# Kernel tuning notes

Hardware: AMD Instinct MI355X
Metric: run time of the kernel (lower is better)

## Reference

```python
import jax, jax.numpy as jnp
import numpy as np

NUM_NODES = 100000
NUM_REL = 237
D = 200            # entity_out_dim_1 * nheads_GAT_1 = 100*2
C = 50             # conv_out_channels
B = 8192           # batch of (h, r, t) triples


def setup_inputs() -> dict:
    key = jax.random.key(0)
    ks = jax.random.split(key, 8)
    heads = jax.random.randint(ks[0], (B, 1), 0, NUM_NODES)
    rels = jax.random.randint(ks[1], (B, 1), 0, NUM_REL)
    tails = jax.random.randint(ks[2], (B, 1), 0, NUM_NODES)
    batch_inputs = jnp.concatenate([heads, rels, tails], axis=1).astype(jnp.int64)
    return {
        "batch_inputs": batch_inputs,
        "final_entity_embeddings": jax.random.normal(ks[3], (NUM_NODES, D), jnp.float32),
        "final_relation_embeddings": jax.random.normal(ks[4], (NUM_REL, D), jnp.float32),
        "W_ent2rel": jax.random.normal(ks[5], (NUM_REL, D, D), jnp.float32) * (1.0 / np.sqrt(D)),
        "conv_w": jax.random.normal(ks[6], (C, 3), jnp.float32) * 0.5,
        "conv_b": jnp.zeros((C,), jnp.float32),
        "fc_w": jax.random.normal(ks[7], (1, C * D), jnp.float32) * (1.0 / np.sqrt(C * D)),
        "fc_b": jnp.zeros((1,), jnp.float32),
    }


def reference(batch_inputs, final_entity_embeddings, final_relation_embeddings,
              W_ent2rel, conv_w, conv_b, fc_w, fc_b):
    h_idx, r_idx, t_idx = batch_inputs[:, 0], batch_inputs[:, 1], batch_inputs[:, 2]
    src = final_entity_embeddings[h_idx]        # [B, D]
    rel = final_relation_embeddings[r_idx]      # [B, D]
    tail = final_entity_embeddings[t_idx]       # [B, D]
    W = W_ent2rel[r_idx]                        # [B, D, D] per-edge relation transform
    # bmm([B,1,D], [B,D,D]) -> [B,1,D], nonlinearity_ent2rel = tanh
    src = jnp.tanh(jnp.einsum('bd,bde->be', src, W))
    tail = jnp.tanh(jnp.einsum('bd,bde->be', tail, W))
    # ConvKB: stack triple as length-3 sequence, Conv2d kernel (1,3) over seq
    stacked = jnp.stack([src, rel, tail], axis=1)            # [B, 3, D]
    conv = jnp.einsum('bkd,ck->bcd', stacked, conv_w) + conv_b[None, :, None]
    conv = jax.nn.relu(conv)                                  # dropout p=0.0 (eval)
    flat = conv.reshape(conv.shape[0], -1)                    # [B, C*D] (C-major, matches torch view)
    out = flat @ fc_w.T + fc_b                                # [B, 1]
    return out
```

## Files before the change

### kernel.cpp

```cpp
#include <hip/hip_runtime.h>
#include <hip/hip_bf16.h>
#include <math.h>

#define DDIM 200
#define D4   50
#define CCH  50
#define NREL 237
#define MAXE 4
#define MAXR 8
#define AROWS 16
#define NT   256
#define KT   7
#define KTKG 28
#define NCOLP 208
#define OSTRIDE 204
#define PACK_UNITS (NREL * KTKG * NCOLP)

typedef __attribute__((ext_vector_type(8))) short bf16x8;
typedef __attribute__((ext_vector_type(4))) float f32x4;

__device__ __forceinline__ uint f2bf(float x) {
    __hip_bfloat16 h = __float2bfloat16(x);
    return (uint)*reinterpret_cast<ushort*>(&h);
}

__device__ __forceinline__ float fast_tanh(float x) {
    const float xc = fminf(fmaxf(x, -20.f), 20.f);
    const float e  = __expf(2.f * xc);
    return 1.f - __fdividef(2.f, e + 1.f);
}

__global__ __launch_bounds__(1024) void prep_kernel(
    const float* __restrict__ W, ushort* __restrict__ Wpk, int do_pack,
    const int* __restrict__ bi, int B, int nblk,
    int* __restrict__ perm, int* __restrict__ blk_r,
    int* __restrict__ blk_start, int* __restrict__ blk_cnt)
{
    const int tid = threadIdx.x;

    if (blockIdx.x != 0) {
        if (!do_pack) return;
        const int u = (blockIdx.x - 1) * 1024 + tid;
        if (u >= PACK_UNITS) return;
        const int col  = u % NCOLP;
        const int rk   = u / NCOLP;
        const int ktkg = rk % KTKG;
        const int r    = rk / KTKG;
        const int k0   = ktkg * 8;
        uint4 pk = {0u, 0u, 0u, 0u};
        if (col < DDIM) {
            const float* base = W + (size_t)r * DDIM * DDIM + col;
            uint vv[8];
            #pragma unroll
            for (int j = 0; j < 8; ++j) {
                const int k = k0 + j;
                vv[j] = (k < DDIM) ? f2bf(base[(size_t)k * DDIM]) : 0u;
            }
            pk.x = vv[0] | (vv[1] << 16);
            pk.y = vv[2] | (vv[3] << 16);
            pk.z = vv[4] | (vv[5] << 16);
            pk.w = vv[6] | (vv[7] << 16);
        }
        *(uint4*)&Wpk[(size_t)u * 8] = pk;
        return;
    }

    __shared__ int hist[NREL];
    __shared__ int offs[NREL];
    __shared__ int wsum[16], wsum2[16];
    const int lane = tid & 63;
    const int w    = tid >> 6;

    if (tid < NREL) hist[tid] = 0;
    __syncthreads();
    for (int i = tid; i < B; i += 1024)
        atomicAdd(&hist[bi[i * 3 + 1]], 1);
    __syncthreads();

    const int v  = (tid < NREL) ? hist[tid] : 0;
    const int v2 = (tid < NREL) ? (v + MAXE - 1) / MAXE : 0;
    int s = v, s2 = v2;
    #pragma unroll
    for (int off = 1; off < 64; off <<= 1) {
        const int u  = __shfl_up(s,  off, 64);
        const int u2 = __shfl_up(s2, off, 64);
        if (lane >= off) { s += u; s2 += u2; }
    }
    if (lane == 63) { wsum[w] = s; wsum2[w] = s2; }
    __syncthreads();
    int base = 0, base2 = 0;
    for (int i = 0; i < w; ++i) { base += wsum[i]; base2 += wsum2[i]; }
    const int my_off  = base  + s  - v;
    const int my_boff = base2 + s2 - v2;
    if (tid < NREL) offs[tid] = my_off;
    __syncthreads();

    for (int i = tid; i < nblk; i += 1024) blk_cnt[i] = 0;
    if (tid < NREL && v > 0) {
        const int nb = (v + MAXE - 1) / MAXE;
        const int cb = v / nb, ext = v - cb * nb;
        int pos = my_off;
        for (int j = 0; j < nb; ++j) {
            const int c = cb + (j < ext ? 1 : 0);
            blk_r[my_boff + j]     = tid;
            blk_start[my_boff + j] = pos;
            blk_cnt[my_boff + j]   = c;
            pos += c;
        }
    }
    __syncthreads();
    for (int i = tid; i < B; i += 1024) {
        const int pos = atomicAdd(&offs[bi[i * 3 + 1]], 1);
        perm[pos] = i;
    }
}

template <bool PACKED>
__global__ __launch_bounds__(NT) void spkbgat_mfma_kernel(
    const int*   __restrict__ bi,
    const float* __restrict__ ent,
    const float* __restrict__ rel_emb,
    const float* __restrict__ W,
    const ushort* __restrict__ Wpk,
    const float* __restrict__ conv_w,
    const float* __restrict__ conv_b,
    const float* __restrict__ fc_w,
    const float* __restrict__ fc_b,
    const int*   __restrict__ perm,
    const int*   __restrict__ blk_r,
    const int*   __restrict__ blk_start,
    const int*   __restrict__ blk_cnt,
    int nblk,
    float*       __restrict__ out)
{
    __shared__ __align__(16) ushort Ash[KTKG * AROWS * 8];
    __shared__ __align__(16) float  Osh[MAXR][OSTRIDE];
    __shared__ __align__(16) float4 rl4[D4];
    __shared__ __align__(16) float  cwb[CCH][4];
    __shared__ int eid_lds[MAXR];
    __shared__ int bix_lds[MAXE];

    const int tid  = threadIdx.x;
    const int w    = tid >> 6;
    const int lane = tid & 63;
    const int l16  = lane & 15;
    const int kg   = lane >> 4;

    const int bid = blockIdx.x;
    const int q = nblk >> 3, rmd = nblk & 7;
    const int xcd = bid & 7, idx = bid >> 3;
    const int gidx = (xcd < rmd ? xcd * (q + 1) : rmd * (q + 1) + (xcd - rmd) * q) + idx;

    const int cnt = blk_cnt[gidx];
    if (cnt == 0) return;

    const int r     = blk_r[gidx];
    const int start = blk_start[gidx];
    const int rows  = 2 * cnt;

    if (tid < CCH) {
        cwb[tid][0] = conv_w[tid * 3 + 0];
        cwb[tid][1] = conv_w[tid * 3 + 1];
        cwb[tid][2] = conv_w[tid * 3 + 2];
        cwb[tid][3] = conv_b[tid];
    }
    if (tid < D4) rl4[tid] = ((const float4*)rel_emb)[r * D4 + tid];
    if (tid < MAXE) {
        const int b = (tid < cnt) ? perm[start + tid] : -1;
        bix_lds[tid] = b;
        const int bb = (b >= 0) ? b : 0;
        eid_lds[2 * tid]     = bi[3 * bb + 0];
        eid_lds[2 * tid + 1] = bi[3 * bb + 2];
    }
    __syncthreads();

    for (int u = tid; u < KTKG * AROWS; u += NT) {
        const int row  = u & (AROWS - 1);
        const int ktkg = u >> 4;
        uint4 pk = {0u, 0u, 0u, 0u};
        if (ktkg < 25 && row < rows) {
            const float* xp = ent + (size_t)eid_lds[row] * DDIM + ktkg * 8;
            const float4 x0 = *(const float4*)xp;
            const float4 x1 = *(const float4*)(xp + 4);
            pk.x = f2bf(x0.x) | (f2bf(x0.y) << 16);
            pk.y = f2bf(x0.z) | (f2bf(x0.w) << 16);
            pk.z = f2bf(x1.x) | (f2bf(x1.y) << 16);
            pk.w = f2bf(x1.z) | (f2bf(x1.w) << 16);
        }
        *(uint4*)&Ash[u * 8] = pk;
    }
    __syncthreads();

    const int nslots = (w == 0) ? 4 : 3;
    const float*  __restrict__ Wr = W + (size_t)r * DDIM * DDIM;
    const ushort* __restrict__ Wp = Wpk + (size_t)r * KTKG * NCOLP * 8;
    f32x4 acc[4];
    #pragma unroll
    for (int s = 0; s < 4; ++s) acc[s] = (f32x4){0.f, 0.f, 0.f, 0.f};

    for (int kt = 0; kt < KT; ++kt) {
        const int ktkg = kt * 4 + kg;
        const bf16x8 a0 = *(const bf16x8*)&Ash[(ktkg * AROWS + l16) * 8];
        #pragma unroll
        for (int s = 0; s < 4; ++s) {
            if (s < nslots) {
                const int col = (w + 4 * s) * 16 + l16;
                bf16x8 bf;
                if (PACKED) {
                    bf = *(const bf16x8*)&Wp[((size_t)ktkg * NCOLP + col) * 8];
                } else {
                    const int k0 = ktkg * 8;
                    #pragma unroll
                    for (int j = 0; j < 8; ++j) {
                        const int k = k0 + j;
                        const float vv = (k < DDIM && col < DDIM) ? Wr[k * DDIM + col] : 0.f;
                        bf[j] = (short)f2bf(vv);
                    }
                }
                acc[s] = __builtin_amdgcn_mfma_f32_16x16x32_bf16(a0, bf, acc[s], 0, 0, 0);
            }
        }
    }

    #pragma unroll
    for (int s = 0; s < 4; ++s) {
        if (s < nslots) {
            const int gcol = (w + 4 * s) * 16 + l16;
            if (gcol < DDIM) {
                #pragma unroll
                for (int v = 0; v < 4; ++v) {
                    const int grow = kg * 4 + v;
                    if (grow < rows)
                        Osh[grow][gcol] = fast_tanh(acc[s][v]);
                }
            }
        }
    }
    __syncthreads();

    float4 sumv = {0.f, 0.f, 0.f, 0.f};
    const bool live = (w < cnt);
    if (lane < D4 && live) {
        const float4 rv = rl4[lane];
        const float4 se = *(const float4*)&Osh[2 * w][4 * lane];
        const float4 te = *(const float4*)&Osh[2 * w + 1][4 * lane];
        for (int c = 0; c < CCH; ++c) {
            const float4 cw  = *(const float4*)&cwb[c][0];
            const float4 fc4 = ((const float4*)fc_w)[c * D4 + lane];
            const float v0 = fmaf(cw.x, se.x, fmaf(cw.y, rv.x, fmaf(cw.z, te.x, cw.w)));
            const float v1 = fmaf(cw.x, se.y, fmaf(cw.y, rv.y, fmaf(cw.z, te.y, cw.w)));
            const float v2 = fmaf(cw.x, se.z, fmaf(cw.y, rv.z, fmaf(cw.z, te.z, cw.w)));
            const float v3 = fmaf(cw.x, se.w, fmaf(cw.y, rv.w, fmaf(cw.z, te.w, cw.w)));
            sumv.x = fmaf(fmaxf(v0, 0.f), fc4.x, sumv.x);
            sumv.y = fmaf(fmaxf(v1, 0.f), fc4.y, sumv.y);
            sumv.z = fmaf(fmaxf(v2, 0.f), fc4.z, sumv.z);
            sumv.w = fmaf(fmaxf(v3, 0.f), fc4.w, sumv.w);
        }
    }
    float sum = (sumv.x + sumv.y) + (sumv.z + sumv.w);
    #pragma unroll
    for (int off = 32; off; off >>= 1)
        sum += __shfl_down(sum, off, 64);
    if (lane == 0 && live) out[bix_lds[w]] = sum + fc_b[0];
}

extern "C" void kernel_launch(void* const* d_in, const int* in_sizes, int n_in,
                              void* d_out, int out_size, void* d_ws, size_t ws_size,
                              hipStream_t stream) {
    const int*   bi      = (const int*)  d_in[0];
    const float* ent     = (const float*)d_in[1];
    const float* rel_emb = (const float*)d_in[2];
    const float* W       = (const float*)d_in[3];
    const float* conv_w  = (const float*)d_in[4];
    const float* conv_b  = (const float*)d_in[5];
    const float* fc_w    = (const float*)d_in[6];
    const float* fc_b    = (const float*)d_in[7];
    float*       out     = (float*)d_out;

    const int B    = in_sizes[0] / 3;
    const int nblk = NREL + (B + MAXE - 1) / MAXE;

    int* perm      = (int*)d_ws;
    int* blk_r     = perm + B;
    int* blk_start = blk_r + nblk;
    int* blk_cnt   = blk_start + nblk;

    const size_t meta_bytes = (size_t)(B + 3 * nblk) * sizeof(int);
    const size_t pk_off     = (meta_bytes + 255) & ~(size_t)255;
    const size_t need       = pk_off + (size_t)PACK_UNITS * 16;
    const bool   use_packed = (ws_size >= need);
    ushort* Wpk = (ushort*)((char*)d_ws + pk_off);

    const int prep_blocks = 1 + (PACK_UNITS + 1023) / 1024;
    prep_kernel<<<prep_blocks, 1024, 0, stream>>>(
        W, Wpk, use_packed ? 1 : 0, bi, B, nblk, perm, blk_r, blk_start, blk_cnt);

    if (use_packed) {
        spkbgat_mfma_kernel<true><<<nblk, NT, 0, stream>>>(
            bi, ent, rel_emb, W, Wpk, conv_w, conv_b, fc_w, fc_b,
            perm, blk_r, blk_start, blk_cnt, nblk, out);
    } else {
        spkbgat_mfma_kernel<false><<<nblk, NT, 0, stream>>>(
            bi, ent, rel_emb, W, Wpk, conv_w, conv_b, fc_w, fc_b,
            perm, blk_r, blk_start, blk_cnt, nblk, out);
    }
}
```

Before: 57.41 us.

## Split fused GEMM+epilogue into separate GEMM and epilogue kernels with larger tiles

Splits the per-relation kernel into two. The GEMM kernel now handles up to 16 triples (32 rows, two MFMA M-tiles) per block, loads entity rows straight into registers instead of staging them in LDS, and writes the tanh outputs as bf16 to a workspace buffer. A new epilogue kernel stages fc_w in LDS and computes the ConvKB reduction for two triples per wave. The aim is to load each relation's W slice fewer times, cut the number of blocks, and drop the per-block global fc_w reads. In exchange it adds a kernel launch, a global round trip for the intermediates, and a bf16 rounding step on the tanh outputs.

```diff
diff --git a/kernel.cpp b/kernel.cpp
--- a/kernel.cpp
+++ b/kernel.cpp
@@ -6,15 +6,14 @@
 #define D4   50
 #define CCH  50
 #define NREL 237
-#define MAXE 4
-#define MAXR 8
-#define AROWS 16
+#define MAXE 16
 #define NT   256
 #define KT   7
 #define KTKG 28
 #define NCOLP 208
-#define OSTRIDE 204
+#define ZSTR 208
 #define PACK_UNITS (NREL * KTKG * NCOLP)
+#define EPB_EPI 8
 
 typedef __attribute__((ext_vector_type(8))) short bf16x8;
 typedef __attribute__((ext_vector_type(4))) float f32x4;
@@ -23,7 +22,9 @@
     __hip_bfloat16 h = __float2bfloat16(x);
     return (uint)*reinterpret_cast<ushort*>(&h);
 }
-
+__device__ __forceinline__ float bf2f(ushort u) {
+    return __uint_as_float((uint)u << 16);
+}
 __device__ __forceinline__ float fast_tanh(float x) {
     const float xc = fminf(fmaxf(x, -20.f), 20.f);
     const float e  = __expf(2.f * xc);
@@ -34,7 +35,8 @@
     const float* __restrict__ W, ushort* __restrict__ Wpk, int do_pack,
     const int* __restrict__ bi, int B, int nblk,
     int* __restrict__ perm, int* __restrict__ blk_r,
-    int* __restrict__ blk_start, int* __restrict__ blk_cnt)
+    int* __restrict__ blk_start, int* __restrict__ blk_cnt,
+    int* __restrict__ eidArr, int* __restrict__ prb, int* __restrict__ prr)
 {
     const int tid = threadIdx.x;
 
@@ -113,33 +115,28 @@
         const int pos = atomicAdd(&offs[bi[i * 3 + 1]], 1);
         perm[pos] = i;
     }
+    __syncthreads();
+    for (int p = tid; p < B; p += 1024) {
+        const int b = perm[p];
+        eidArr[2 * p]     = bi[3 * b + 0];
+        eidArr[2 * p + 1] = bi[3 * b + 2];
+        prb[p] = b;
+        prr[p] = bi[3 * b + 1];
+    }
 }
 
 template <bool PACKED>
-__global__ __launch_bounds__(NT) void spkbgat_mfma_kernel(
-    const int*   __restrict__ bi,
-    const float* __restrict__ ent,
-    const float* __restrict__ rel_emb,
-    const float* __restrict__ W,
+__global__ __launch_bounds__(NT) void gemm_kernel(
+    const float*  __restrict__ ent,
+    const float*  __restrict__ W,
     const ushort* __restrict__ Wpk,
-    const float* __restrict__ conv_w,
-    const float* __restrict__ conv_b,
-    const float* __restrict__ fc_w,
-    const float* __restrict__ fc_b,
-    const int*   __restrict__ perm,
-    const int*   __restrict__ blk_r,
-    const int*   __restrict__ blk_start,
-    const int*   __restrict__ blk_cnt,
+    const int*    __restrict__ blk_r,
+    const int*    __restrict__ blk_start,
+    const int*    __restrict__ blk_cnt,
+    const int*    __restrict__ eidArr,
     int nblk,
-    float*       __restrict__ out)
+    ushort*       __restrict__ Zpk)
 {
-    __shared__ __align__(16) ushort Ash[KTKG * AROWS * 8];
-    __shared__ __align__(16) float  Osh[MAXR][OSTRIDE];
-    __shared__ __align__(16) float4 rl4[D4];
-    __shared__ __align__(16) float  cwb[CCH][4];
-    __shared__ int eid_lds[MAXR];
-    __shared__ int bix_lds[MAXE];
-
     const int tid  = threadIdx.x;
     const int w    = tid >> 6;
     const int lane = tid & 63;
@@ -153,115 +150,178 @@
 
     const int cnt = blk_cnt[gidx];
     if (cnt == 0) return;
-
     const int r     = blk_r[gidx];
     const int start = blk_start[gidx];
     const int rows  = 2 * cnt;
 
+    const int row0 = l16, row1 = 16 + l16;
+    const int e0 = (row0 < rows) ? eidArr[2 * start + row0] : 0;
+    const int e1 = (row1 < rows) ? eidArr[2 * start + row1] : 0;
+    const float* __restrict__ xp0 = ent + (size_t)e0 * DDIM;
+    const float* __restrict__ xp1 = ent + (size_t)e1 * DDIM;
+
+    const ushort* __restrict__ Wp = Wpk + (size_t)r * KTKG * NCOLP * 8;
+    const float*  __restrict__ Wr = W + (size_t)r * DDIM * DDIM;
+    const int nslots = (w == 0) ? 4 : 3;
+
+    f32x4 acc[2][4];
+    #pragma unroll
+    for (int mt = 0; mt < 2; ++mt)
+        #pragma unroll
+        for (int s = 0; s < 4; ++s)
+            acc[mt][s] = (f32x4){0.f, 0.f, 0.f, 0.f};
+
+    #pragma unroll 2
+    for (int kt = 0; kt < KT; ++kt) {
+        const int ktkg = kt * 4 + kg;
+        const int k0   = ktkg * 8;
+        uint4 pa0 = {0u, 0u, 0u, 0u}, pa1 = {0u, 0u, 0u, 0u};
+        if (ktkg < 25) {
+            const float4 a = *(const float4*)(xp0 + k0);
+            const float4 b = *(const float4*)(xp0 + k0 + 4);
+            pa0.x = f2bf(a.x) | (f2bf(a.y) << 16);
+            pa0.y = f2bf(a.z) | (f2bf(a.w) << 16);
+            pa0.z = f2bf(b.x) | (f2bf(b.y) << 16);
+            pa0.w = f2bf(b.z) | (f2bf(b.w) << 16);
+            const float4 c = *(const float4*)(xp1 + k0);
+            const float4 d = *(const float4*)(xp1 + k0 + 4);
+            pa1.x = f2bf(c.x) | (f2bf(c.y) << 16);
+            pa1.y = f2bf(c.z) | (f2bf(c.w) << 16);
+            pa1.z = f2bf(d.x) | (f2bf(d.y) << 16);
+            pa1.w = f2bf(d.z) | (f2bf(d.w) << 16);
+        }
+        const bf16x8 a0 = *reinterpret_cast<const bf16x8*>(&pa0);
+        const bf16x8 a1 = *reinterpret_cast<const bf16x8*>(&pa1);
+        #pragma unroll
+        for (int s = 0; s < 4; ++s) {
+            if (s < nslots) {
+                const int col = (w + 4 * s) * 16 + l16;
+                bf16x8 bfr;
+                if (PACKED) {
+                    bfr = *(const bf16x8*)&Wp[((size_t)ktkg * NCOLP + col) * 8];
+                } else {
+                    #pragma unroll
+                    for (int j = 0; j < 8; ++j) {
+                        const int k = k0 + j;
+                        const float vv = (k < DDIM && col < DDIM) ? Wr[k * DDIM + col] : 0.f;
+                        bfr[j] = (short)f2bf(vv);
+                    }
+                }
+                acc[0][s] = __builtin_amdgcn_mfma_f32_16x16x32_bf16(a0, bfr, acc[0][s], 0, 0, 0);
+                acc[1][s] = __builtin_amdgcn_mfma_f32_16x16x32_bf16(a1, bfr, acc[1][s], 0, 0, 0);
+            }
+        }
+    }
+
+    #pragma unroll
+    for (int mt = 0; mt < 2; ++mt) {
+        #pragma unroll
+        for (int s = 0; s < 4; ++s) {
+            if (s < nslots) {
+                const int col = (w + 4 * s) * 16 + l16;
+                #pragma unroll
+                for (int v = 0; v < 4; ++v) {
+                    const int grow = 16 * mt + kg * 4 + v;
+                    if (grow < rows)
+                        Zpk[(size_t)(2 * start + grow) * ZSTR + col] =
+                            (ushort)f2bf(fast_tanh(acc[mt][s][v]));
+                }
+            }
+        }
+    }
+}
+
+__global__ __launch_bounds__(NT) void epi_kernel(
+    const ushort* __restrict__ Zpk,
+    const float*  __restrict__ rel_emb,
+    const float*  __restrict__ conv_w,
+    const float*  __restrict__ conv_b,
+    const float*  __restrict__ fc_w,
+    const float*  __restrict__ fc_b,
+    const int*    __restrict__ prb,
+    const int*    __restrict__ prr,
+    int B,
+    float*        __restrict__ out)
+{
+    __shared__ __align__(16) float4 fsh[CCH * D4];
+    __shared__ __align__(16) float  cwb[CCH][4];
+
+    const int tid  = threadIdx.x;
+    const int w    = tid >> 6;
+    const int lane = tid & 63;
+
+    for (int i = tid; i < CCH * D4; i += NT) fsh[i] = ((const float4*)fc_w)[i];
     if (tid < CCH) {
         cwb[tid][0] = conv_w[tid * 3 + 0];
         cwb[tid][1] = conv_w[tid * 3 + 1];
         cwb[tid][2] = conv_w[tid * 3 + 2];
         cwb[tid][3] = conv_b[tid];
     }
-    if (tid < D4) rl4[tid] = ((const float4*)rel_emb)[r * D4 + tid];
-    if (tid < MAXE) {
-        const int b = (tid < cnt) ? perm[start + tid] : -1;
-        bix_lds[tid] = b;
-        const int bb = (b >= 0) ? b : 0;
-        eid_lds[2 * tid]     = bi[3 * bb + 0];
-        eid_lds[2 * tid + 1] = bi[3 * bb + 2];
-    }
-    __syncthreads();
-
-    for (int u = tid; u < KTKG * AROWS; u += NT) {
-        const int row  = u & (AROWS - 1);
-        const int ktkg = u >> 4;
-        uint4 pk = {0u, 0u, 0u, 0u};
-        if (ktkg < 25 && row < rows) {
-            const float* xp = ent + (size_t)eid_lds[row] * DDIM + ktkg * 8;
-            const float4 x0 = *(const float4*)xp;
-            const float4 x1 = *(const float4*)(xp + 4);
-            pk.x = f2bf(x0.x) | (f2bf(x0.y) << 16);
-            pk.y = f2bf(x0.z) | (f2bf(x0.w) << 16);
-            pk.z = f2bf(x1.x) | (f2bf(x1.y) << 16);
-            pk.w = f2bf(x1.z) | (f2bf(x1.w) << 16);
-        }
-        *(uint4*)&Ash[u * 8] = pk;
-    }
-    __syncthreads();
-
-    const int nslots = (w == 0) ? 4 : 3;
-    const float*  __restrict__ Wr = W + (size_t)r * DDIM * DDIM;
-    const ushort* __restrict__ Wp = Wpk + (size_t)r * KTKG * NCOLP * 8;
-    f32x4 acc[4];
+    __syncthreads();
+
+    const int p0 = blockIdx.x * EPB_EPI + w * 2;
+    const int p1 = p0 + 1;
+    const bool l0 = (p0 < B), l1 = (p1 < B);
+    const int b0 = l0 ? prb[p0] : 0;
+    const int b1 = l1 ? prb[p1] : 0;
+    const int r0 = l0 ? prr[p0] : 0;
+    const int r1 = l1 ? prr[p1] : 0;
+
+    float4 a0 = {0.f, 0.f, 0.f, 0.f}, a1 = {0.f, 0.f, 0.f, 0.f};
+    if (lane < D4) {
+        float4 se0 = {0,0,0,0}, te0 = {0,0,0,0}, rv0 = {0,0,0,0};
+        float4 se1 = {0,0,0,0}, te1 = {0,0,0,0}, rv1 = {0,0,0,0};
+        if (l0) {
+            rv0 = *(const float4*)&rel_emb[r0 * DDIM + 4 * lane];
+            const ushort4 su = *(const ushort4*)&Zpk[(size_t)(2 * p0) * ZSTR + 4 * lane];
+            const ushort4 tu = *(const ushort4*)&Zpk[(size_t)(2 * p0 + 1) * ZSTR + 4 * lane];
+            se0 = (float4){bf2f(su.x), bf2f(su.y), bf2f(su.z), bf2f(su.w)};
+            te0 = (float4){bf2f(tu.x), bf2f(tu.y), bf2f(tu.z), bf2f(tu.w)};
+        }
+        if (l1) {
+            rv1 = *(const float4*)&rel_emb[r1 * DDIM + 4 * lane];
+            const ushort4 su = *(const ushort4*)&Zpk[(size_t)(2 * p1) * ZSTR + 4 * lane];
+            const ushort4 tu = *(const ushort4*)&Zpk[(size_t)(2 * p1 + 1) * ZSTR + 4 * lane];
+            se1 = (float4){bf2f(su.x), bf2f(su.y), bf2f(su.z), bf2f(su.w)};
+            te1 = (float4){bf2f(tu.x), bf2f(tu.y), bf2f(tu.z), bf2f(tu.w)};
+        }
+        for (int c = 0; c < CCH; ++c) {
+            const float4 cw = *(const float4*)&cwb[c][0];
+            const float4 f4 = fsh[c * D4 + lane];
+            {
+                const float v0 = fmaf(cw.x, se0.x, fmaf(cw.y, rv0.x, fmaf(cw.z, te0.x, cw.w)));
+                const float v1 = fmaf(cw.x, se0.y, fmaf(cw.y, rv0.y, fmaf(cw.z, te0.y, cw.w)));
+                const float v2 = fmaf(cw.x, se0.z, fmaf(cw.y, rv0.z, fmaf(cw.z, te0.z, cw.w)));
+                const float v3 = fmaf(cw.x, se0.w, fmaf(cw.y, rv0.w, fmaf(cw.z, te0.w, cw.w)));
+                a0.x = fmaf(fmaxf(v0, 0.f), f4.x, a0.x);
+                a0.y = fmaf(fmaxf(v1, 0.f), f4.y, a0.y);
+                a0.z = fmaf(fmaxf(v2, 0.f), f4.z, a0.z);
+                a0.w = fmaf(fmaxf(v3, 0.f), f4.w, a0.w);
+            }
+            {
+                const float v0 = fmaf(cw.x, se1.x, fmaf(cw.y, rv1.x, fmaf(cw.z, te1.x, cw.w)));
+                const float v1 = fmaf(cw.x, se1.y, fmaf(cw.y, rv1.y, fmaf(cw.z, te1.y, cw.w)));
+                const float v2 = fmaf(cw.x, se1.z, fmaf(cw.y, rv1.z, fmaf(cw.z, te1.z, cw.w)));
+                const float v3 = fmaf(cw.x, se1.w, fmaf(cw.y, rv1.w, fmaf(cw.z, te1.w, cw.w)));
+                a1.x = fmaf(fmaxf(v0, 0.f), f4.x, a1.x);
+                a1.y = fmaf(fmaxf(v1, 0.f), f4.y, a1.y);
+                a1.z = fmaf(fmaxf(v2, 0.f), f4.z, a1.z);
+                a1.w = fmaf(fmaxf(v3, 0.f), f4.w, a1.w);
+            }
+        }
+    }
+    float s0 = (a0.x + a0.y) + (a0.z + a0.w);
+    float s1 = (a1.x + a1.y) + (a1.z + a1.w);
     #pragma unroll
-    for (int s = 0; s < 4; ++s) acc[s] = (f32x4){0.f, 0.f, 0.f, 0.f};
-
-    for (int kt = 0; kt < KT; ++kt) {
-        const int ktkg = kt * 4 + kg;
-        const bf16x8 a0 = *(const bf16x8*)&Ash[(ktkg * AROWS + l16) * 8];
-        #pragma unroll
-        for (int s = 0; s < 4; ++s) {
-            if (s < nslots) {
-                const int col = (w + 4 * s) * 16 + l16;
-                bf16x8 bf;
-                if (PACKED) {
-                    bf = *(const bf16x8*)&Wp[((size_t)ktkg * NCOLP + col) * 8];
-                } else {
-                    const int k0 = ktkg * 8;
-                    #pragma unroll
-                    for (int j = 0; j < 8; ++j) {
-                        const int k = k0 + j;
-                        const float vv = (k < DDIM && col < DDIM) ? Wr[k * DDIM + col] : 0.f;
-                        bf[j] = (short)f2bf(vv);
-                    }
-                }
-                acc[s] = __builtin_amdgcn_mfma_f32_16x16x32_bf16(a0, bf, acc[s], 0, 0, 0);
-            }
-        }
-    }
-
-    #pragma unroll
-    for (int s = 0; s < 4; ++s) {
-        if (s < nslots) {
-            const int gcol = (w + 4 * s) * 16 + l16;
-            if (gcol < DDIM) {
-                #pragma unroll
-                for (int v = 0; v < 4; ++v) {
-                    const int grow = kg * 4 + v;
-                    if (grow < rows)
-                        Osh[grow][gcol] = fast_tanh(acc[s][v]);
-                }
-            }
-        }
-    }
-    __syncthreads();
-
-    float4 sumv = {0.f, 0.f, 0.f, 0.f};
-    const bool live = (w < cnt);
-    if (lane < D4 && live) {
-        const float4 rv = rl4[lane];
-        const float4 se = *(const float4*)&Osh[2 * w][4 * lane];
-        const float4 te = *(const float4*)&Osh[2 * w + 1][4 * lane];
-        for (int c = 0; c < CCH; ++c) {
-            const float4 cw  = *(const float4*)&cwb[c][0];
-            const float4 fc4 = ((const float4*)fc_w)[c * D4 + lane];
-            const float v0 = fmaf(cw.x, se.x, fmaf(cw.y, rv.x, fmaf(cw.z, te.x, cw.w)));
-            const float v1 = fmaf(cw.x, se.y, fmaf(cw.y, rv.y, fmaf(cw.z, te.y, cw.w)));
-            const float v2 = fmaf(cw.x, se.z, fmaf(cw.y, rv.z, fmaf(cw.z, te.z, cw.w)));
-            const float v3 = fmaf(cw.x, se.w, fmaf(cw.y, rv.w, fmaf(cw.z, te.w, cw.w)));
-            sumv.x = fmaf(fmaxf(v0, 0.f), fc4.x, sumv.x);
-            sumv.y = fmaf(fmaxf(v1, 0.f), fc4.y, sumv.y);
-            sumv.z = fmaf(fmaxf(v2, 0.f), fc4.z, sumv.z);
-            sumv.w = fmaf(fmaxf(v3, 0.f), fc4.w, sumv.w);
-        }
-    }
-    float sum = (sumv.x + sumv.y) + (sumv.z + sumv.w);
-    #pragma unroll
-    for (int off = 32; off; off >>= 1)
-        sum += __shfl_down(sum, off, 64);
-    if (lane == 0 && live) out[bix_lds[w]] = sum + fc_b[0];
+    for (int off = 32; off; off >>= 1) {
+        s0 += __shfl_down(s0, off, 64);
+        s1 += __shfl_down(s1, off, 64);
+    }
+    if (lane == 0) {
+        const float fb = fc_b[0];
+        if (l0) out[b0] = s0 + fb;
+        if (l1) out[b1] = s1 + fb;
+    }
 }
 
 extern "C" void kernel_launch(void* const* d_in, const int* in_sizes, int n_in,
@@ -284,24 +344,32 @@
     int* blk_r     = perm + B;
     int* blk_start = blk_r + nblk;
     int* blk_cnt   = blk_start + nblk;
-
-    const size_t meta_bytes = (size_t)(B + 3 * nblk) * sizeof(int);
-    const size_t pk_off     = (meta_bytes + 255) & ~(size_t)255;
+    int* eidArr    = blk_cnt + nblk;
+    int* prb       = eidArr + 2 * B;
+    int* prr       = prb + B;
+
+    const size_t meta_bytes = (size_t)(5 * B + 3 * nblk) * sizeof(int);
+    const size_t z_off      = (meta_bytes + 255) & ~(size_t)255;
+    const size_t z_bytes    = (size_t)2 * B * ZSTR * sizeof(ushort);
+    const size_t pk_off     = (z_off + z_bytes + 255) & ~(size_t)255;
     const size_t need       = pk_off + (size_t)PACK_UNITS * 16;
     const bool   use_packed = (ws_size >= need);
+    ushort* Zpk = (ushort*)((char*)d_ws + z_off);
     ushort* Wpk = (ushort*)((char*)d_ws + pk_off);
 
     const int prep_blocks = 1 + (PACK_UNITS + 1023) / 1024;
     prep_kernel<<<prep_blocks, 1024, 0, stream>>>(
-        W, Wpk, use_packed ? 1 : 0, bi, B, nblk, perm, blk_r, blk_start, blk_cnt);
+        W, Wpk, use_packed ? 1 : 0, bi, B, nblk,
+        perm, blk_r, blk_start, blk_cnt, eidArr, prb, prr);
 
     if (use_packed) {
-        spkbgat_mfma_kernel<true><<<nblk, NT, 0, stream>>>(
-            bi, ent, rel_emb, W, Wpk, conv_w, conv_b, fc_w, fc_b,
-            perm, blk_r, blk_start, blk_cnt, nblk, out);
+        gemm_kernel<true><<<nblk, NT, 0, stream>>>(
+            ent, W, Wpk, blk_r, blk_start, blk_cnt, eidArr, nblk, Zpk);
     } else {
-        spkbgat_mfma_kernel<false><<<nblk, NT, 0, stream>>>(
-            bi, ent, rel_emb, W, Wpk, conv_w, conv_b, fc_w, fc_b,
-            perm, blk_r, blk_start, blk_cnt, nblk, out);
-    }
-}
+        gemm_kernel<false><<<nblk, NT, 0, stream>>>(
+            ent, W, Wpk, blk_r, blk_start, blk_cnt, eidArr, nblk, Zpk);
+    }
+
+    epi_kernel<<<(B + EPB_EPI - 1) / EPB_EPI, NT, 0, stream>>>(
+        Zpk, rel_emb, conv_w, conv_b, fc_w, fc_b, prb, prr, B, out);
+}
```

Result: slower. 62.99 us (+9.7%).

## Double edges per block, pre-gather entity ids, prefetch packed W fragments

Applied to the files above, without the earlier changes.

Raises the per-block edge count from 4 to 8 so all 16 MFMA A rows are used. This halves the number of blocks and doubles reuse of each packed relation-weight tile. The prep kernel now writes a sorted array of head/tail entity ids, which removes the per-block perm/bi indirection and one __syncthreads. The MFMA loop keeps all A fragments in registers and double-buffers the B fragment loads. The epilogue handles two edges per wave. The costs are higher register pressure, fewer blocks (less parallelism across CUs), and a serial extra pass over B in the single-block part of prep.

```diff
diff --git a/kernel.cpp b/kernel.cpp
--- a/kernel.cpp
+++ b/kernel.cpp
@@ -6,8 +6,7 @@
 #define D4   50
 #define CCH  50
 #define NREL 237
-#define MAXE 4
-#define MAXR 8
+#define MAXE 8
 #define AROWS 16
 #define NT   256
 #define KT   7
@@ -23,7 +22,6 @@
     __hip_bfloat16 h = __float2bfloat16(x);
     return (uint)*reinterpret_cast<ushort*>(&h);
 }
-
 __device__ __forceinline__ float fast_tanh(float x) {
     const float xc = fminf(fmaxf(x, -20.f), 20.f);
     const float e  = __expf(2.f * xc);
@@ -34,7 +32,8 @@
     const float* __restrict__ W, ushort* __restrict__ Wpk, int do_pack,
     const int* __restrict__ bi, int B, int nblk,
     int* __restrict__ perm, int* __restrict__ blk_r,
-    int* __restrict__ blk_start, int* __restrict__ blk_cnt)
+    int* __restrict__ blk_start, int* __restrict__ blk_cnt,
+    int* __restrict__ eidArr)
 {
     const int tid = threadIdx.x;
 
@@ -113,32 +112,36 @@
         const int pos = atomicAdd(&offs[bi[i * 3 + 1]], 1);
         perm[pos] = i;
     }
+    __syncthreads();
+    for (int p = tid; p < B; p += 1024) {
+        const int b = perm[p];
+        eidArr[2 * p]     = bi[3 * b + 0];
+        eidArr[2 * p + 1] = bi[3 * b + 2];
+    }
 }
 
 template <bool PACKED>
 __global__ __launch_bounds__(NT) void spkbgat_mfma_kernel(
-    const int*   __restrict__ bi,
-    const float* __restrict__ ent,
-    const float* __restrict__ rel_emb,
-    const float* __restrict__ W,
+    const float*  __restrict__ ent,
+    const float*  __restrict__ rel_emb,
+    const float*  __restrict__ W,
     const ushort* __restrict__ Wpk,
-    const float* __restrict__ conv_w,
-    const float* __restrict__ conv_b,
-    const float* __restrict__ fc_w,
-    const float* __restrict__ fc_b,
-    const int*   __restrict__ perm,
-    const int*   __restrict__ blk_r,
-    const int*   __restrict__ blk_start,
-    const int*   __restrict__ blk_cnt,
+    const float*  __restrict__ conv_w,
+    const float*  __restrict__ conv_b,
+    const float*  __restrict__ fc_w,
+    const float*  __restrict__ fc_b,
+    const int*    __restrict__ perm,
+    const int*    __restrict__ blk_r,
+    const int*    __restrict__ blk_start,
+    const int*    __restrict__ blk_cnt,
+    const int*    __restrict__ eidArr,
     int nblk,
-    float*       __restrict__ out)
+    float*        __restrict__ out)
 {
     __shared__ __align__(16) ushort Ash[KTKG * AROWS * 8];
-    __shared__ __align__(16) float  Osh[MAXR][OSTRIDE];
+    __shared__ __align__(16) float  Osh[AROWS][OSTRIDE];
     __shared__ __align__(16) float4 rl4[D4];
     __shared__ __align__(16) float  cwb[CCH][4];
-    __shared__ int eid_lds[MAXR];
-    __shared__ int bix_lds[MAXE];
 
     const int tid  = threadIdx.x;
     const int w    = tid >> 6;
@@ -165,21 +168,14 @@
         cwb[tid][3] = conv_b[tid];
     }
     if (tid < D4) rl4[tid] = ((const float4*)rel_emb)[r * D4 + tid];
-    if (tid < MAXE) {
-        const int b = (tid < cnt) ? perm[start + tid] : -1;
-        bix_lds[tid] = b;
-        const int bb = (b >= 0) ? b : 0;
-        eid_lds[2 * tid]     = bi[3 * bb + 0];
-        eid_lds[2 * tid + 1] = bi[3 * bb + 2];
-    }
-    __syncthreads();
 
     for (int u = tid; u < KTKG * AROWS; u += NT) {
         const int row  = u & (AROWS - 1);
         const int ktkg = u >> 4;
         uint4 pk = {0u, 0u, 0u, 0u};
         if (ktkg < 25 && row < rows) {
-            const float* xp = ent + (size_t)eid_lds[row] * DDIM + ktkg * 8;
+            const int eid = eidArr[2 * start + row];
+            const float* xp = ent + (size_t)eid * DDIM + ktkg * 8;
             const float4 x0 = *(const float4*)xp;
             const float4 x1 = *(const float4*)(xp + 4);
             pk.x = f2bf(x0.x) | (f2bf(x0.y) << 16);
@@ -193,31 +189,59 @@
 
     const int nslots = (w == 0) ? 4 : 3;
     const float*  __restrict__ Wr = W + (size_t)r * DDIM * DDIM;
-    const ushort* __restrict__ Wp = Wpk + (size_t)r * KTKG * NCOLP * 8;
+    const ushort* __restrict__ Wp0 = Wpk + (size_t)r * KTKG * NCOLP * 8
+                                   + ((size_t)kg * NCOLP) * 8 + (size_t)l16 * 8;
+
+    bf16x8 a_frag[KT];
+    #pragma unroll
+    for (int kt = 0; kt < KT; ++kt)
+        a_frag[kt] = *(const bf16x8*)&Ash[((kt * 4 + kg) * AROWS + l16) * 8];
+
     f32x4 acc[4];
     #pragma unroll
     for (int s = 0; s < 4; ++s) acc[s] = (f32x4){0.f, 0.f, 0.f, 0.f};
 
-    for (int kt = 0; kt < KT; ++kt) {
-        const int ktkg = kt * 4 + kg;
-        const bf16x8 a0 = *(const bf16x8*)&Ash[(ktkg * AROWS + l16) * 8];
+    if (PACKED) {
+        bf16x8 bcur[4], bnxt[4];
         #pragma unroll
-        for (int s = 0; s < 4; ++s) {
-            if (s < nslots) {
-                const int col = (w + 4 * s) * 16 + l16;
-                bf16x8 bf;
-                if (PACKED) {
-                    bf = *(const bf16x8*)&Wp[((size_t)ktkg * NCOLP + col) * 8];
-                } else {
-                    const int k0 = ktkg * 8;
+        for (int s = 0; s < 4; ++s)
+            if (s < nslots)
+                bcur[s] = *(const bf16x8*)(Wp0 + (size_t)(w + 4 * s) * 16 * 8);
+        #pragma unroll
+        for (int kt = 0; kt < KT; ++kt) {
+            if (kt + 1 < KT) {
+                const ushort* pn = Wp0 + (size_t)(kt + 1) * 4 * NCOLP * 8;
+                #pragma unroll
+                for (int s = 0; s < 4; ++s)
+                    if (s < nslots)
+                        bnxt[s] = *(const bf16x8*)(pn + (size_t)(w + 4 * s) * 16 * 8);
+            }
+            #pragma unroll
+            for (int s = 0; s < 4; ++s)
+                if (s < nslots)
+                    acc[s] = __builtin_amdgcn_mfma_f32_16x16x32_bf16(
+                        a_frag[kt], bcur[s], acc[s], 0, 0, 0);
+            #pragma unroll
+            for (int s = 0; s < 4; ++s)
+                if (s < nslots) bcur[s] = bnxt[s];
+        }
+    } else {
+        for (int kt = 0; kt < KT; ++kt) {
+            const int k0b = (kt * 4 + kg) * 8;
+            #pragma unroll
+            for (int s = 0; s < 4; ++s) {
+                if (s < nslots) {
+                    const int col = (w + 4 * s) * 16 + l16;
+                    bf16x8 bfr;
                     #pragma unroll
                     for (int j = 0; j < 8; ++j) {
-                        const int k = k0 + j;
+                        const int k = k0b + j;
                         const float vv = (k < DDIM && col < DDIM) ? Wr[k * DDIM + col] : 0.f;
-                        bf[j] = (short)f2bf(vv);
+                        bfr[j] = (short)f2bf(vv);
                     }
+                    acc[s] = __builtin_amdgcn_mfma_f32_16x16x32_bf16(
+                        a_frag[kt], bfr, acc[s], 0, 0, 0);
                 }
-                acc[s] = __builtin_amdgcn_mfma_f32_16x16x32_bf16(a0, bf, acc[s], 0, 0, 0);
             }
         }
     }
@@ -238,30 +262,47 @@
     }
     __syncthreads();
 
-    float4 sumv = {0.f, 0.f, 0.f, 0.f};
-    const bool live = (w < cnt);
-    if (lane < D4 && live) {
+    float4 sa[2] = {{0,0,0,0}, {0,0,0,0}};
+    if (lane < D4) {
         const float4 rv = rl4[lane];
-        const float4 se = *(const float4*)&Osh[2 * w][4 * lane];
-        const float4 te = *(const float4*)&Osh[2 * w + 1][4 * lane];
+        float4 se[2], te[2];
+        #pragma unroll
+        for (int s2 = 0; s2 < 2; ++s2) {
+            const int e = w + 4 * s2;
+            if (e < cnt) {
+                se[s2] = *(const float4*)&Osh[2 * e][4 * lane];
+                te[s2] = *(const float4*)&Osh[2 * e + 1][4 * lane];
+            } else {
+                se[s2] = (float4){0,0,0,0};
+                te[s2] = (float4){0,0,0,0};
+            }
+        }
         for (int c = 0; c < CCH; ++c) {
             const float4 cw  = *(const float4*)&cwb[c][0];
             const float4 fc4 = ((const float4*)fc_w)[c * D4 + lane];
-            const float v0 = fmaf(cw.x, se.x, fmaf(cw.y, rv.x, fmaf(cw.z, te.x, cw.w)));
-            const float v1 = fmaf(cw.x, se.y, fmaf(cw.y, rv.y, fmaf(cw.z, te.y, cw.w)));
-            const float v2 = fmaf(cw.x, se.z, fmaf(cw.y, rv.z, fmaf(cw.z, te.z, cw.w)));
-            const float v3 = fmaf(cw.x, se.w, fmaf(cw.y, rv.w, fmaf(cw.z, te.w, cw.w)));
-            sumv.x = fmaf(fmaxf(v0, 0.f), fc4.x, sumv.x);
-            sumv.y = fmaf(fmaxf(v1, 0.f), fc4.y, sumv.y);
-            sumv.z = fmaf(fmaxf(v2, 0.f), fc4.z, sumv.z);
-            sumv.w = fmaf(fmaxf(v3, 0.f), fc4.w, sumv.w);
-        }
-    }
-    float sum = (sumv.x + sumv.y) + (sumv.z + sumv.w);
-    #pragma unroll
-    for (int off = 32; off; off >>= 1)
-        sum += __shfl_down(sum, off, 64);
-    if (lane == 0 && live) out[bix_lds[w]] = sum + fc_b[0];
+            #pragma unroll
+            for (int s2 = 0; s2 < 2; ++s2) {
+                const float v0 = fmaf(cw.x, se[s2].x, fmaf(cw.y, rv.x, fmaf(cw.z, te[s2].x, cw.w)));
+                const float v1 = fmaf(cw.x, se[s2].y, fmaf(cw.y, rv.y, fmaf(cw.z, te[s2].y, cw.w)));
+                const float v2 = fmaf(cw.x, se[s2].z, fmaf(cw.y, rv.z, fmaf(cw.z, te[s2].z, cw.w)));
+                const float v3 = fmaf(cw.x, se[s2].w, fmaf(cw.y, rv.w, fmaf(cw.z, te[s2].w, cw.w)));
+                sa[s2].x = fmaf(fmaxf(v0, 0.f), fc4.x, sa[s2].x);
+                sa[s2].y = fmaf(fmaxf(v1, 0.f), fc4.y, sa[s2].y);
+                sa[s2].z = fmaf(fmaxf(v2, 0.f), fc4.z, sa[s2].z);
+                sa[s2].w = fmaf(fmaxf(v3, 0.f), fc4.w, sa[s2].w);
+            }
+        }
+    }
+    #pragma unroll
+    for (int s2 = 0; s2 < 2; ++s2) {
+        float sum = (sa[s2].x + sa[s2].y) + (sa[s2].z + sa[s2].w);
+        #pragma unroll
+        for (int off = 32; off; off >>= 1)
+            sum += __shfl_down(sum, off, 64);
+        const int e = w + 4 * s2;
+        if (lane == 0 && e < cnt)
+            out[perm[start + e]] = sum + fc_b[0];
+    }
 }
 
 extern "C" void kernel_launch(void* const* d_in, const int* in_sizes, int n_in,
@@ -284,8 +325,9 @@
     int* blk_r     = perm + B;
     int* blk_start = blk_r + nblk;
     int* blk_cnt   = blk_start + nblk;
-
-    const size_t meta_bytes = (size_t)(B + 3 * nblk) * sizeof(int);
+    int* eidArr    = blk_cnt + nblk;
+
+    const size_t meta_bytes = (size_t)(3 * B + 3 * nblk) * sizeof(int);
     const size_t pk_off     = (meta_bytes + 255) & ~(size_t)255;
     const size_t need       = pk_off + (size_t)PACK_UNITS * 16;
     const bool   use_packed = (ws_size >= need);
@@ -293,15 +335,16 @@
 
     const int prep_blocks = 1 + (PACK_UNITS + 1023) / 1024;
     prep_kernel<<<prep_blocks, 1024, 0, stream>>>(
-        W, Wpk, use_packed ? 1 : 0, bi, B, nblk, perm, blk_r, blk_start, blk_cnt);
+        W, Wpk, use_packed ? 1 : 0, bi, B, nblk,
+        perm, blk_r, blk_start, blk_cnt, eidArr);
 
     if (use_packed) {
         spkbgat_mfma_kernel<true><<<nblk, NT, 0, stream>>>(
-            bi, ent, rel_emb, W, Wpk, conv_w, conv_b, fc_w, fc_b,
-            perm, blk_r, blk_start, blk_cnt, nblk, out);
+            ent, rel_emb, W, Wpk, conv_w, conv_b, fc_w, fc_b,
+            perm, blk_r, blk_start, blk_cnt, eidArr, nblk, out);
     } else {
         spkbgat_mfma_kernel<false><<<nblk, NT, 0, stream>>>(
-            bi, ent, rel_emb, W, Wpk, conv_w, conv_b, fc_w, fc_b,
-            perm, blk_r, blk_start, blk_cnt, nblk, out);
-    }
-}
+            ent, rel_emb, W, Wpk, conv_w, conv_b, fc_w, fc_b,
+            perm, blk_r, blk_start, blk_cnt, eidArr, nblk, out);
+    }
+}
```

Result: no change. 58.50 us (+1.9%).
